# Performance work log

Measured on AMD Instinct MI355X. Metric: run time of the kernel, lower is better.

Reference implementation:

```python
import jax, jax.numpy as jnp
import numpy as np

NUM_GRAPHS = 100_000
NODES_PER_GRAPH = 38
NUM_NODES = NUM_GRAPHS * NODES_PER_GRAPH
NUM_EDGES = 60_800_000


def setup_inputs() -> dict:
    key = jax.random.key(0)
    ks = jax.random.split(key, 12)
    x = jax.random.normal(ks[0], (NUM_NODES, 1), dtype=jnp.float32)
    edge_index = jax.random.randint(ks[1], (2, NUM_EDGES), 0, NUM_NODES, dtype=jnp.int32)
    edge_attr = jax.random.normal(ks[2], (NUM_EDGES, 1), dtype=jnp.float32)
    # NNConv(1, 1, Linear(1, 1), aggr='add') params
    conv_root = jax.random.normal(ks[3], (1, 1), dtype=jnp.float32)
    conv_bias = jax.random.normal(ks[4], (1,), dtype=jnp.float32) * 0.1
    edge_nn_w = jax.random.normal(ks[5], (1, 1), dtype=jnp.float32)
    edge_nn_b = jax.random.normal(ks[6], (1,), dtype=jnp.float32) * 0.1
    # dense head params: 38 -> 4 -> 4 -> 1
    W1 = jax.random.normal(ks[7], (38, 4), dtype=jnp.float32) * (1.0 / np.sqrt(38))
    b1 = jax.random.normal(ks[8], (4,), dtype=jnp.float32) * 0.1
    W2 = jax.random.normal(ks[9], (4, 4), dtype=jnp.float32) * 0.5
    b2 = jax.random.normal(ks[10], (4,), dtype=jnp.float32) * 0.1
    W3 = jax.random.normal(ks[11], (4, 1), dtype=jnp.float32) * 0.5
    b3 = jnp.zeros((1,), dtype=jnp.float32)
    return {"x": x, "edge_index": edge_index, "edge_attr": edge_attr,
            "conv_root": conv_root, "conv_bias": conv_bias,
            "edge_nn_w": edge_nn_w, "edge_nn_b": edge_nn_b,
            "W1": W1, "b1": b1, "W2": W2, "b2": b2, "W3": W3, "b3": b3}


def reference(x, edge_index, edge_attr, conv_root, conv_bias,
              edge_nn_w, edge_nn_b, W1, b1, W2, b2, W3, b3):
    src, dst = edge_index[0], edge_index[1]  # messages flow src -> dst
    # edge-conditioned weight: Linear(1,1) on edge_attr -> [E,1] (in*out = 1)
    w_e = edge_attr @ edge_nn_w + edge_nn_b            # [E, 1]
    msg = x[src] * w_e                                  # gather + per-edge scale, [E, 1]
    agg = jax.ops.segment_sum(msg, dst, num_segments=NUM_NODES)  # scatter-add, [N, 1]
    nodes = x @ conv_root + agg + conv_bias             # [N, 1]
    h = nodes.reshape(NUM_GRAPHS, NODES_PER_GRAPH)      # [G, 38]
    h = jax.nn.relu(h @ W1 + b1)
    h = jax.nn.relu(h @ W2 + b2)
    out = jax.nn.sigmoid(h @ W3 + b3) * 11.0            # [G, 1]
    return out
```

## Files before the change

### kernel.cpp

```cpp
#include <hip/hip_runtime.h>
#include <hip/hip_fp16.h>
#include <math.h>

constexpr int NG  = 100000;
constexpr int NPG = 38;
constexpr int NN  = NG * NPG;
constexpr long long NE = 60800000LL;

constexpr int BIN_SHIFT = 14;
constexpr int BINW      = 1 << BIN_SHIFT;
constexpr int NB        = (NN + BINW - 1) / BINW;

constexpr int NR    = 4;
constexpr int I4_R  = (int)(NE / 4 / NR);
constexpr int NBLK1 = 1000;
constexpr int I4_B  = I4_R / NBLK1;
constexpr int CHUNK = 4096;
constexpr int CH_I4 = CHUNK / 4;

constexpr int CAPS1 = 68096;
constexpr int CAPD  = 267264;
constexpr int NB2   = 4;

constexpr size_t AGG_BYTES  = (size_t)NN * 4;
constexpr size_t XH_OFF     = AGG_BYTES;
constexpr size_t XH_BYTES   = (size_t)NB * BINW * 2;
constexpr size_t CUR1_OFF   = XH_OFF + XH_BYTES;
constexpr size_t CUR2_OFF   = CUR1_OFF + 1024;
constexpr size_t REG1_OFF   = ((CUR2_OFF + 1024 + 255) / 256) * 256;
constexpr size_t REG1_BYTES = (size_t)NB * CAPS1 * 8;
constexpr size_t REG2_OFF   = REG1_OFF + REG1_BYTES;
constexpr size_t REG2_BYTES = (size_t)NB * CAPD * 4;
constexpr size_t WS_NEEDED  = REG2_OFF + REG2_BYTES;

__global__ void __launch_bounds__(256) xcast_kernel(
    const float* __restrict__ x, __half2* __restrict__ xh2)
{
    const int i = blockIdx.x * 256 + threadIdx.x;
    if (i < NN / 4) {
        float4 v = ((const float4*)x)[i];
        xh2[2 * i + 0] = __floats2half2_rn(v.x, v.y);
        xh2[2 * i + 1] = __floats2half2_rn(v.z, v.w);
    }
}

__global__ void __launch_bounds__(512) p1_kernel(
    const int*   __restrict__ ei,
    const float* __restrict__ ea,
    const float* __restrict__ wptr,
    const float* __restrict__ bptr,
    unsigned long long* __restrict__ reg1,
    int* __restrict__ cur1,
    int roff)
{
    __shared__ unsigned long long sbuf[CHUNK];
    __shared__ unsigned char     sbin[CHUNK];
    __shared__ int s_scan[256];
    __shared__ int gofs[NB];

    const int t = threadIdx.x;
    if (t < 256) s_scan[t] = 0;
    __syncthreads();

    const float w = wptr[0], b = bptr[0];
    const int4*   src4 = (const int4*)ei + roff + (size_t)blockIdx.x * I4_B;
    const int4*   dst4 = (const int4*)(ei + NE) + roff + (size_t)blockIdx.x * I4_B;
    const float4* ea4  = (const float4*)ea + roff + (size_t)blockIdx.x * I4_B;

    for (int c0 = 0; c0 < I4_B; c0 += CH_I4) {
        const int n4 = min(CH_I4, I4_B - c0);
        int rbin[8]; unsigned long long rpk[8]; int rpos[8];
        #pragma unroll
        for (int u = 0; u < 2; ++u) {
            const int j = u * 512 + t;
            const bool act = j < n4;
            int4   s4 = act ? src4[c0 + j] : make_int4(0, 0, 0, 0);
            int4   d4 = act ? dst4[c0 + j] : make_int4(0, 0, 0, 0);
            float4 e4 = act ? ea4[c0 + j]  : make_float4(0.f, 0.f, 0.f, 0.f);
            int   ss[4] = {s4.x, s4.y, s4.z, s4.w};
            int   dd[4] = {d4.x, d4.y, d4.z, d4.w};
            float ee[4] = {e4.x, e4.y, e4.z, e4.w};
            #pragma unroll
            for (int k = 0; k < 4; ++k) {
                const int idx = u * 4 + k;
                if (act) {
                    const int bin = ss[k] >> BIN_SHIFT;
                    __half_raw hr = __float2half_rn(ee[k] * w + b);
                    rbin[idx] = bin;
                    rpk[idx]  = ((unsigned long long)(unsigned)(ss[k] & (BINW - 1)) << 38)
                              | ((unsigned long long)(unsigned)dd[k] << 16)
                              | (unsigned long long)(unsigned short)hr.x;
                    rpos[idx] = atomicAdd(&s_scan[bin], 1);
                } else { rbin[idx] = -1; rpk[idx] = 0; rpos[idx] = 0; }
            }
        }
        __syncthreads();

        int acc = 0;
        if (t < 256) acc = s_scan[t];
        for (int off = 1; off < 256; off <<= 1) {
            int tmp = 0;
            if (t < 256 && t >= off) tmp = s_scan[t - off];
            __syncthreads();
            if (t < 256) { acc += tmp; s_scan[t] = acc; }
            __syncthreads();
        }

        if (t < NB) {
            const int excl = (t == 0) ? 0 : s_scan[t - 1];
            const int rl   = s_scan[t] - excl;
            gofs[t] = (rl > 0) ? atomicAdd(&cur1[t], rl) : 0;
        }
        #pragma unroll
        for (int k = 0; k < 8; ++k) {
            if (rbin[k] >= 0) {
                const int excl = (rbin[k] == 0) ? 0 : s_scan[rbin[k] - 1];
                const int idx  = excl + rpos[k];
                sbuf[idx] = rpk[k];
                sbin[idx] = (unsigned char)rbin[k];
            }
        }
        __syncthreads();

        const int tot = n4 * 4;
        for (int k = t; k < tot; k += 512) {
            const unsigned long long r = sbuf[k];
            const int bin  = sbin[k];
            const int excl = (bin == 0) ? 0 : s_scan[bin - 1];
            reg1[(size_t)bin * CAPS1 + gofs[bin] + (k - excl)] = r;
        }
        __syncthreads();
        if (t < 256) s_scan[t] = 0;
        __syncthreads();
    }
}

__global__ void __launch_bounds__(512) p2_kernel(
    const __half* __restrict__ xh,
    const unsigned long long* __restrict__ reg1,
    const int* __restrict__ cur1,
    unsigned int* __restrict__ reg2,
    int* __restrict__ cur2)
{
    __shared__ __half        xsl[BINW];
    __shared__ unsigned int  sbuf[CHUNK];
    __shared__ unsigned char sbin[CHUNK];
    __shared__ int s_scan[256];
    __shared__ int gofs[NB];

    const int t  = threadIdx.x;
    const int sb = blockIdx.x >> 2;
    const int jb = blockIdx.x & 3;

    {
        const uint4* s = (const uint4*)(xh + (size_t)sb * BINW);
        uint4* d = (uint4*)xsl;
        for (int i = t; i < BINW / 8; i += 512) d[i] = s[i];
    }
    if (t < 256) s_scan[t] = 0;
    __syncthreads();

    const int n2    = cur1[sb];
    const int cpb   = (n2 + NB2 - 1) / NB2;
    const int start = jb * cpb;
    const int end   = min(start + cpb, n2);
    const unsigned long long* seg = reg1 + (size_t)sb * CAPS1;

    for (int c0 = start; c0 < end; c0 += CHUNK) {
        const int cnt = min(CHUNK, end - c0);
        int rbin[8]; unsigned int rpk[8]; int rpos[8];
        #pragma unroll
        for (int u = 0; u < 8; ++u) {
            const int j = u * 512 + t;
            if (j < cnt) {
                const unsigned long long r = seg[c0 + j];
                const int srclow        = (int)(r >> 38);
                const unsigned int dst  = (unsigned int)(r >> 16) & 0x3FFFFFu;
                __half_raw hm; hm.x = (unsigned short)(r & 0xFFFFu);
                const float msg = __half2float(xsl[srclow]) * __half2float(__half(hm));
                __half_raw ho = __float2half_rn(msg);
                const int bin = (int)(dst >> BIN_SHIFT);
                rbin[u] = bin;
                rpk[u]  = ((dst & (unsigned)(BINW - 1)) << 16) | (unsigned int)(unsigned short)ho.x;
                rpos[u] = atomicAdd(&s_scan[bin], 1);
            } else { rbin[u] = -1; rpk[u] = 0; rpos[u] = 0; }
        }
        __syncthreads();

        int acc = 0;
        if (t < 256) acc = s_scan[t];
        for (int off = 1; off < 256; off <<= 1) {
            int tmp = 0;
            if (t < 256 && t >= off) tmp = s_scan[t - off];
            __syncthreads();
            if (t < 256) { acc += tmp; s_scan[t] = acc; }
            __syncthreads();
        }

        if (t < NB) {
            const int excl = (t == 0) ? 0 : s_scan[t - 1];
            const int rl   = s_scan[t] - excl;
            gofs[t] = (rl > 0) ? atomicAdd(&cur2[t], rl) : 0;
        }
        #pragma unroll
        for (int u = 0; u < 8; ++u) {
            if (rbin[u] >= 0) {
                const int excl = (rbin[u] == 0) ? 0 : s_scan[rbin[u] - 1];
                const int idx  = excl + rpos[u];
                sbuf[idx] = rpk[u];
                sbin[idx] = (unsigned char)rbin[u];
            }
        }
        __syncthreads();

        for (int k = t; k < cnt; k += 512) {
            const unsigned int r = sbuf[k];
            const int bin  = sbin[k];
            const int excl = (bin == 0) ? 0 : s_scan[bin - 1];
            reg2[(size_t)bin * CAPD + gofs[bin] + (k - excl)] = r;
        }
        __syncthreads();
        if (t < 256) s_scan[t] = 0;
        __syncthreads();
    }
}

__global__ void __launch_bounds__(512) reduce_kernel(
    const unsigned int* __restrict__ reg2,
    const int* __restrict__ cur2,
    float* __restrict__ agg)
{
    __shared__ float acc[BINW];
    const int t = threadIdx.x;
    const int b = blockIdx.x;
    for (int i = t; i < BINW; i += 512) acc[i] = 0.0f;
    __syncthreads();

    const int n  = cur2[b];
    const int nb = b << BIN_SHIFT;
    const unsigned int* seg = reg2 + (size_t)b * CAPD;

    int k = t;
    for (; k + 1536 < n; k += 2048) {
        unsigned int r0 = seg[k], r1 = seg[k + 512], r2 = seg[k + 1024], r3 = seg[k + 1536];
        __half_raw h0; h0.x = (unsigned short)(r0 & 0xFFFFu);
        __half_raw h1; h1.x = (unsigned short)(r1 & 0xFFFFu);
        __half_raw h2; h2.x = (unsigned short)(r2 & 0xFFFFu);
        __half_raw h3; h3.x = (unsigned short)(r3 & 0xFFFFu);
        atomicAdd(&acc[r0 >> 16], __half2float(__half(h0)));
        atomicAdd(&acc[r1 >> 16], __half2float(__half(h1)));
        atomicAdd(&acc[r2 >> 16], __half2float(__half(h2)));
        atomicAdd(&acc[r3 >> 16], __half2float(__half(h3)));
    }
    for (; k < n; k += 512) {
        unsigned int r = seg[k];
        __half_raw h; h.x = (unsigned short)(r & 0xFFFFu);
        atomicAdd(&acc[r >> 16], __half2float(__half(h)));
    }
    __syncthreads();

    const int lim = (NN - nb < BINW) ? (NN - nb) : BINW;
    for (int i = t; i < lim; i += 512) agg[nb + i] = acc[i];
}

__global__ void __launch_bounds__(256) edge_kernel(
    const float* __restrict__ x,
    const int*   __restrict__ ei,
    const float* __restrict__ ea,
    const float* __restrict__ wptr,
    const float* __restrict__ bptr,
    float*       __restrict__ agg)
{
    const float w = wptr[0];
    const float b = bptr[0];
    const int nvec = (int)(NE / 4);
    const int4*   src4 = (const int4*)ei;
    const int4*   dst4 = (const int4*)(ei + NE);
    const float4* ea4  = (const float4*)ea;
    const int stride = gridDim.x * blockDim.x;
    for (int i = blockIdx.x * blockDim.x + threadIdx.x; i < nvec; i += stride) {
        int4   s = src4[i];
        int4   d = dst4[i];
        float4 e = ea4[i];
        atomicAdd(&agg[d.x], x[s.x] * (e.x * w + b));
        atomicAdd(&agg[d.y], x[s.y] * (e.y * w + b));
        atomicAdd(&agg[d.z], x[s.z] * (e.z * w + b));
        atomicAdd(&agg[d.w], x[s.w] * (e.w * w + b));
    }
}

__global__ void __launch_bounds__(256) head_kernel(
    const float* __restrict__ x,
    const float* __restrict__ agg,
    const float* __restrict__ conv_root,
    const float* __restrict__ conv_bias,
    const float* __restrict__ W1, const float* __restrict__ b1,
    const float* __restrict__ W2, const float* __restrict__ b2,
    const float* __restrict__ W3, const float* __restrict__ b3,
    float* __restrict__ out)
{
    __shared__ float nv[256 * NPG];
    const float cr = conv_root[0];
    const float cb = conv_bias[0];

    const int gbase = blockIdx.x * 256;
    const int gcount = (NG - gbase < 256) ? (NG - gbase) : 256;
    const int fcount = gcount * NPG;
    const long long nbase = (long long)gbase * NPG;

    for (int k = threadIdx.x; k < fcount; k += 256) {
        long long gi = nbase + k;
        nv[k] = x[gi] * cr + agg[gi] + cb;
    }
    __syncthreads();

    const int g = gbase + threadIdx.x;
    if (g < NG) {
        const float* p = &nv[threadIdx.x * NPG];
        float h0 = b1[0], h1 = b1[1], h2 = b1[2], h3 = b1[3];
        #pragma unroll
        for (int j = 0; j < NPG; ++j) {
            float v = p[j];
            h0 += v * W1[j * 4 + 0];
            h1 += v * W1[j * 4 + 1];
            h2 += v * W1[j * 4 + 2];
            h3 += v * W1[j * 4 + 3];
        }
        h0 = fmaxf(h0, 0.f); h1 = fmaxf(h1, 0.f);
        h2 = fmaxf(h2, 0.f); h3 = fmaxf(h3, 0.f);

        float q0 = b2[0] + h0 * W2[0] + h1 * W2[4] + h2 * W2[8]  + h3 * W2[12];
        float q1 = b2[1] + h0 * W2[1] + h1 * W2[5] + h2 * W2[9]  + h3 * W2[13];
        float q2 = b2[2] + h0 * W2[2] + h1 * W2[6] + h2 * W2[10] + h3 * W2[14];
        float q3 = b2[3] + h0 * W2[3] + h1 * W2[7] + h2 * W2[11] + h3 * W2[15];
        q0 = fmaxf(q0, 0.f); q1 = fmaxf(q1, 0.f);
        q2 = fmaxf(q2, 0.f); q3 = fmaxf(q3, 0.f);

        float z = b3[0] + q0 * W3[0] + q1 * W3[1] + q2 * W3[2] + q3 * W3[3];
        float sgm = 1.0f / (1.0f + __expf(-z));
        out[g] = 11.0f * sgm;
    }
}

extern "C" void kernel_launch(void* const* d_in, const int* in_sizes, int n_in,
                              void* d_out, int out_size, void* d_ws, size_t ws_size,
                              hipStream_t stream) {
    const float* x         = (const float*)d_in[0];
    const int*   ei        = (const int*)  d_in[1];
    const float* ea        = (const float*)d_in[2];
    const float* conv_root = (const float*)d_in[3];
    const float* conv_bias = (const float*)d_in[4];
    const float* ew        = (const float*)d_in[5];
    const float* eb        = (const float*)d_in[6];
    const float* W1        = (const float*)d_in[7];
    const float* b1        = (const float*)d_in[8];
    const float* W2        = (const float*)d_in[9];
    const float* b2        = (const float*)d_in[10];
    const float* W3        = (const float*)d_in[11];
    const float* b3        = (const float*)d_in[12];

    char*  ws  = (char*)d_ws;
    float* agg = (float*)ws;
    float* out = (float*)d_out;

    if (ws_size >= WS_NEEDED) {
        __half*             xh   = (__half*)(ws + XH_OFF);
        int*                cur1 = (int*)(ws + CUR1_OFF);
        int*                cur2 = (int*)(ws + CUR2_OFF);
        unsigned long long* reg1 = (unsigned long long*)(ws + REG1_OFF);
        unsigned int*       reg2 = (unsigned int*)(ws + REG2_OFF);

        xcast_kernel<<<(NN / 4 + 255) / 256, 256, 0, stream>>>(x, (__half2*)xh);
        hipMemsetAsync(cur2, 0, NB * sizeof(int), stream);
        for (int r = 0; r < NR; ++r) {
            hipMemsetAsync(cur1, 0, NB * sizeof(int), stream);
            p1_kernel<<<NBLK1, 512, 0, stream>>>(ei, ea, ew, eb, reg1, cur1, r * I4_R);
            p2_kernel<<<NB * NB2, 512, 0, stream>>>(xh, reg1, cur1, reg2, cur2);
        }
        reduce_kernel<<<NB, 512, 0, stream>>>(reg2, cur2, agg);
    } else {
        hipMemsetAsync(agg, 0, AGG_BYTES, stream);
        edge_kernel<<<2048, 256, 0, stream>>>(x, ei, ea, ew, eb, agg);
    }

    const int hblocks = (NG + 255) / 256;
    head_kernel<<<hblocks, 256, 0, stream>>>(x, agg, conv_root, conv_bias,
                                             W1, b1, W2, b2, W3, b3, out);
}
```

Before: 1.209 ms.

## Split per-bin reduction across multiple blocks and combine partial aggregates

Each bin's reduction is now split across four blocks, each accumulating a quarter of the bin's entries in shared memory and writing its own partial buffer. A new combine kernel sums the four partial buffers into the final aggregate. The goal is more blocks than CUs for better occupancy during reduction, with a wider unroll for more loads in flight. In exchange it adds extra workspace, one more launch and an extra pass over the node array.

```diff
diff --git a/kernel.cpp b/kernel.cpp
--- a/kernel.cpp
+++ b/kernel.cpp
@@ -21,13 +21,17 @@
 constexpr int CAPS1 = 68096;
 constexpr int CAPD  = 267264;
 constexpr int NB2   = 4;
+constexpr int NSPLIT = 4;
 
 constexpr size_t AGG_BYTES  = (size_t)NN * 4;
 constexpr size_t XH_OFF     = AGG_BYTES;
 constexpr size_t XH_BYTES   = (size_t)NB * BINW * 2;
 constexpr size_t CUR1_OFF   = XH_OFF + XH_BYTES;
 constexpr size_t CUR2_OFF   = CUR1_OFF + 1024;
-constexpr size_t REG1_OFF   = ((CUR2_OFF + 1024 + 255) / 256) * 256;
+constexpr size_t PSTRIDE    = (size_t)NB * BINW;
+constexpr size_t PART_OFF   = ((CUR2_OFF + 1024 + 255) / 256) * 256;
+constexpr size_t PART_BYTES = (size_t)NSPLIT * PSTRIDE * 4;
+constexpr size_t REG1_OFF   = PART_OFF + PART_BYTES;
 constexpr size_t REG1_BYTES = (size_t)NB * CAPS1 * 8;
 constexpr size_t REG2_OFF   = REG1_OFF + REG1_BYTES;
 constexpr size_t REG2_BYTES = (size_t)NB * CAPD * 4;
@@ -228,39 +232,61 @@
 __global__ void __launch_bounds__(512) reduce_kernel(
     const unsigned int* __restrict__ reg2,
     const int* __restrict__ cur2,
-    float* __restrict__ agg)
+    float* __restrict__ part_agg)
 {
     __shared__ float acc[BINW];
-    const int t = threadIdx.x;
-    const int b = blockIdx.x;
+    const int t    = threadIdx.x;
+    const int b    = blockIdx.x / NSPLIT;
+    const int part = blockIdx.x % NSPLIT;
     for (int i = t; i < BINW; i += 512) acc[i] = 0.0f;
     __syncthreads();
 
     const int n  = cur2[b];
-    const int nb = b << BIN_SHIFT;
+    const int i0 = (int)(((long long)part * n) / NSPLIT);
+    const int i1 = (int)(((long long)(part + 1) * n) / NSPLIT);
     const unsigned int* seg = reg2 + (size_t)b * CAPD;
 
-    int k = t;
-    for (; k + 1536 < n; k += 2048) {
-        unsigned int r0 = seg[k], r1 = seg[k + 512], r2 = seg[k + 1024], r3 = seg[k + 1536];
-        __half_raw h0; h0.x = (unsigned short)(r0 & 0xFFFFu);
-        __half_raw h1; h1.x = (unsigned short)(r1 & 0xFFFFu);
-        __half_raw h2; h2.x = (unsigned short)(r2 & 0xFFFFu);
-        __half_raw h3; h3.x = (unsigned short)(r3 & 0xFFFFu);
-        atomicAdd(&acc[r0 >> 16], __half2float(__half(h0)));
-        atomicAdd(&acc[r1 >> 16], __half2float(__half(h1)));
-        atomicAdd(&acc[r2 >> 16], __half2float(__half(h2)));
-        atomicAdd(&acc[r3 >> 16], __half2float(__half(h3)));
-    }
-    for (; k < n; k += 512) {
+    int k = i0 + t;
+    for (; k + 3584 < i1; k += 4096) {
+        unsigned int r[8];
+        #pragma unroll
+        for (int u = 0; u < 8; ++u) r[u] = seg[k + u * 512];
+        #pragma unroll
+        for (int u = 0; u < 8; ++u) {
+            __half_raw h; h.x = (unsigned short)(r[u] & 0xFFFFu);
+            atomicAdd(&acc[r[u] >> 16], __half2float(__half(h)));
+        }
+    }
+    for (; k < i1; k += 512) {
         unsigned int r = seg[k];
         __half_raw h; h.x = (unsigned short)(r & 0xFFFFu);
         atomicAdd(&acc[r >> 16], __half2float(__half(h)));
     }
     __syncthreads();
 
-    const int lim = (NN - nb < BINW) ? (NN - nb) : BINW;
-    for (int i = t; i < lim; i += 512) agg[nb + i] = acc[i];
+    float* dst = part_agg + (size_t)part * PSTRIDE + ((size_t)b << BIN_SHIFT);
+    for (int i = t; i < BINW; i += 512) dst[i] = acc[i];
+}
+
+__global__ void __launch_bounds__(256) combine_kernel(
+    const float* __restrict__ part_agg, float* __restrict__ agg)
+{
+    const int stride = gridDim.x * 256;
+    const int n4 = NN / 4;
+    const float4* p0 = (const float4*)(part_agg);
+    const float4* p1 = (const float4*)(part_agg + PSTRIDE);
+    const float4* p2 = (const float4*)(part_agg + 2 * PSTRIDE);
+    const float4* p3 = (const float4*)(part_agg + 3 * PSTRIDE);
+    float4* o = (float4*)agg;
+    for (int i = blockIdx.x * 256 + threadIdx.x; i < n4; i += stride) {
+        float4 a = p0[i], b = p1[i], c = p2[i], d = p3[i];
+        float4 r;
+        r.x = a.x + b.x + c.x + d.x;
+        r.y = a.y + b.y + c.y + d.y;
+        r.z = a.z + b.z + c.z + d.z;
+        r.w = a.w + b.w + c.w + d.w;
+        o[i] = r;
+    }
 }
 
 __global__ void __launch_bounds__(256) edge_kernel(
@@ -364,11 +390,12 @@
     float* out = (float*)d_out;
 
     if (ws_size >= WS_NEEDED) {
-        __half*             xh   = (__half*)(ws + XH_OFF);
-        int*                cur1 = (int*)(ws + CUR1_OFF);
-        int*                cur2 = (int*)(ws + CUR2_OFF);
-        unsigned long long* reg1 = (unsigned long long*)(ws + REG1_OFF);
-        unsigned int*       reg2 = (unsigned int*)(ws + REG2_OFF);
+        __half*             xh    = (__half*)(ws + XH_OFF);
+        int*                cur1  = (int*)(ws + CUR1_OFF);
+        int*                cur2  = (int*)(ws + CUR2_OFF);
+        float*              partp = (float*)(ws + PART_OFF);
+        unsigned long long* reg1  = (unsigned long long*)(ws + REG1_OFF);
+        unsigned int*       reg2  = (unsigned int*)(ws + REG2_OFF);
 
         xcast_kernel<<<(NN / 4 + 255) / 256, 256, 0, stream>>>(x, (__half2*)xh);
         hipMemsetAsync(cur2, 0, NB * sizeof(int), stream);
@@ -377,7 +404,8 @@
             p1_kernel<<<NBLK1, 512, 0, stream>>>(ei, ea, ew, eb, reg1, cur1, r * I4_R);
             p2_kernel<<<NB * NB2, 512, 0, stream>>>(xh, reg1, cur1, reg2, cur2);
         }
-        reduce_kernel<<<NB, 512, 0, stream>>>(reg2, cur2, agg);
+        reduce_kernel<<<NB * NSPLIT, 512, 0, stream>>>(reg2, cur2, partp);
+        combine_kernel<<<2048, 256, 0, stream>>>(partp, agg);
     } else {
         hipMemsetAsync(agg, 0, AGG_BYTES, stream);
         edge_kernel<<<2048, 256, 0, stream>>>(x, ei, ea, ew, eb, agg);
```

New measurement: 1.225 ms. Within noise of the previous version (+1.3%).
